# Performance work log

Hardware: AMD Instinct MI355X
Metric: run time of the kernel (lower is better)

## Reference

```python
import jax, jax.numpy as jnp
import numpy as np

B, S, D, H = 2, 1024, 1024, 8
HD = D // H            # head_dim = 128
NBUCKETS = 64          # bucket_size (number of hash buckets)
NEG = -1e30


def setup_inputs() -> dict:
    key = jax.random.key(0)
    ks = jax.random.split(key, 10)
    scale = D ** -0.5
    return {
        "x": jax.random.normal(ks[0], (B, S, D), dtype=jnp.float32),
        "Wq": jax.random.normal(ks[1], (D, D), dtype=jnp.float32) * scale,
        "bq": jnp.zeros((D,), dtype=jnp.float32),
        "Wk": jax.random.normal(ks[2], (D, D), dtype=jnp.float32) * scale,
        "bk": jnp.zeros((D,), dtype=jnp.float32),
        "Wv": jax.random.normal(ks[3], (D, D), dtype=jnp.float32) * scale,
        "bv": jnp.zeros((D,), dtype=jnp.float32),
        "Wo": jax.random.normal(ks[4], (D, D), dtype=jnp.float32) * scale,
        "bo": jnp.zeros((D,), dtype=jnp.float32),
        "hash_proj": jax.random.normal(ks[5], (H, HD, NBUCKETS), dtype=jnp.float32),
    }


def reference(x, Wq, bq, Wk, bk, Wv, bv, Wo, bo, hash_proj):
    b, s, d = x.shape
    n = b * s  # buckets gather (batch, token) pairs jointly -> flatten batch into tokens

    def split_heads(y):  # [B,S,D] -> [H, B*S, HD]
        return y.reshape(b, s, H, HD).transpose(2, 0, 1, 3).reshape(H, n, HD)

    q = split_heads(x @ Wq + bq)
    k = split_heads(x @ Wk + bk)
    v = split_heads(x @ Wv + bv)

    # learned LSH routing: argmax over hash projections per head
    hash_scores = jnp.einsum('hnd,hdf->hnf', q, hash_proj)
    buckets = jnp.argmax(hash_scores, axis=-1)  # [H, N] int

    # per-bucket attention == masked dense attention with same-bucket mask
    dots = jnp.einsum('hnd,hmd->hnm', q, k) / (HD ** 0.5)  # [H,N,N]
    same = buckets[:, :, None] == buckets[:, None, :]
    attn = jax.nn.softmax(jnp.where(same, dots, NEG), axis=-1)
    o = jnp.einsum('hnm,hmd->hnd', attn, v)  # [H,N,HD]

    out = o.reshape(H, b, s, HD).transpose(1, 2, 0, 3).reshape(b, s, d)
    return out @ Wo + bo
```

## Files before the change

kernel.cpp:

```cpp
#include <hip/hip_runtime.h>
#include <stdint.h>

typedef __attribute__((ext_vector_type(8))) short short8;
typedef __attribute__((ext_vector_type(4))) short short4v;
typedef __attribute__((ext_vector_type(4))) float float4v;
typedef unsigned short u16;

#define N_TOK 2048
#define D_MODEL 1024
#define N_HEAD 8
#define HDIM 128
#define N_BUCKET 64
#define WL_CAP 2048
#define ATTN_BLOCKS 384

__device__ __forceinline__ u16 f2bf(float f) {
  uint32_t u = __float_as_uint(f);
  uint32_t r = u + 0x7fffu + ((u >> 16) & 1u);
  return (u16)(r >> 16);
}
__device__ __forceinline__ float bf2f(u16 h) {
  return __uint_as_float(((uint32_t)h) << 16);
}

__device__ __forceinline__ void async_load16(const void* g, void* l) {
  __builtin_amdgcn_global_load_lds(
      (const __attribute__((address_space(1))) void*)g,
      (__attribute__((address_space(3))) void*)l, 16, 0, 0);
}

__device__ __forceinline__ int xcd_swz(int bid, int nwg) {
  return (bid & 7) * (nwg >> 3) + (bid >> 3);
}

__global__ __launch_bounds__(256) void prep_kernel(
    const float* __restrict__ x, const float* __restrict__ Wq,
    const float* __restrict__ Wk, const float* __restrict__ Wv,
    const float* __restrict__ Wo, const float* __restrict__ proj,
    u16* __restrict__ xhi, u16* __restrict__ xlo,
    u16* __restrict__ wqt_hi, u16* __restrict__ wqt_lo, u16* __restrict__ kvt,
    u16* __restrict__ wot, u16* __restrict__ projt_hi,
    u16* __restrict__ projt_lo) {
  const int z = blockIdx.z;
  if (z == 4) {
    int base = (blockIdx.y * 32 + blockIdx.x) * 2048 + threadIdx.x * 8;
    float4v a = *(const float4v*)&x[base];
    float4v b = *(const float4v*)&x[base + 4];
    short8 hi, lo;
#pragma unroll
    for (int j = 0; j < 4; j++) {
      u16 h = f2bf(a[j]);
      hi[j] = (short)h;
      lo[j] = (short)f2bf(a[j] - bf2f(h));
    }
#pragma unroll
    for (int j = 0; j < 4; j++) {
      u16 h = f2bf(b[j]);
      hi[4 + j] = (short)h;
      lo[4 + j] = (short)f2bf(b[j] - bf2f(h));
    }
    *(short8*)&xhi[base] = hi;
    *(short8*)&xlo[base] = lo;
    return;
  }
  __shared__ float tile[32][33];
  int tx = threadIdx.x & 31, ty = threadIdx.x >> 5;
  if (z == 5) {
    if (blockIdx.x >= 2) return;
    const int head = blockIdx.y >> 2;
    const int r0 = (blockIdx.y & 3) * 32;
    const int c0 = blockIdx.x * 32;
    const float* in = proj + (size_t)head * 128 * 64;
#pragma unroll
    for (int i = 0; i < 4; i++) {
      int rl = ty + i * 8;
      tile[rl][tx] = in[(size_t)(r0 + rl) * 64 + c0 + tx];
    }
    __syncthreads();
#pragma unroll
    for (int i = 0; i < 4; i++) {
      int cl = ty + i * 8;
      float v = tile[tx][cl];
      size_t oidx = (size_t)head * 64 * 128 + (size_t)(c0 + cl) * 128 + r0 + tx;
      u16 h = f2bf(v);
      projt_hi[oidx] = h;
      projt_lo[oidx] = f2bf(v - bf2f(h));
    }
    return;
  }
  const float* in = (z == 0) ? Wq : (z == 1) ? Wk : (z == 2) ? Wv : Wo;
  u16* hi = (z == 0) ? wqt_hi
            : (z == 1) ? kvt
            : (z == 2) ? (kvt + (size_t)1024 * 1024) : wot;
  u16* lo = (z == 0) ? wqt_lo : nullptr;
  const int C = 1024, R = 1024;
  int c0 = blockIdx.x * 32, r0 = blockIdx.y * 32;
#pragma unroll
  for (int i = 0; i < 4; i++) {
    int rl = ty + i * 8;
    tile[rl][tx] = in[(size_t)(r0 + rl) * C + c0 + tx];
  }
  __syncthreads();
#pragma unroll
  for (int i = 0; i < 4; i++) {
    int cl = ty + i * 8;
    float v = tile[tx][cl];
    size_t oidx = (size_t)(c0 + cl) * R + r0 + tx;
    u16 h = f2bf(v);
    hi[oidx] = h;
    if (lo) lo[oidx] = f2bf(v - bf2f(h));
  }
}

template <int BM>
__device__ __forceinline__ void stage_tiles2(const u16* A, const u16* Bt,
                                             u16* As, u16* Bs, int bm, int bn,
                                             int K, int ko, int wave, int lane) {
  const int arow = lane >> 2;
  const int acolb = (lane & 3) * 16;
  constexpr int ACH = BM / 16;
  constexpr int PC = (ACH + 8) / 4;
#pragma unroll
  for (int cc = 0; cc < PC; cc++) {
    int idx = wave * PC + cc;
    if (idx < ACH) {
      int row = idx * 16 + arow;
      const char* g = (const char*)A + ((size_t)(bm + row) * K + ko) * 2 + acolb;
      async_load16(g, (char*)As + idx * 1024);
    } else {
      int row = (idx - ACH) * 16 + arow;
      const char* g = (const char*)Bt + ((size_t)(bn + row) * K + ko) * 2 + acolb;
      async_load16(g, (char*)Bs + (idx - ACH) * 1024);
    }
  }
}

template <int BM>
__global__ __launch_bounds__(256) void gemm_bf16_kernel(
    const u16* __restrict__ A, const u16* __restrict__ Bt,
    float* __restrict__ C, const float* __restrict__ bias,
    const float* __restrict__ bias2, u16* __restrict__ kbf,
    u16* __restrict__ vbf, int N, int K, int flags) {
  constexpr int MI = BM / 32;
  __shared__ __align__(16) u16 As[2][BM * 32];
  __shared__ __align__(16) u16 Bs[2][128 * 32];
  const int tid = threadIdx.x;
  const int wave = tid >> 6, lane = tid & 63;
  const int lhi = lane >> 4, llo = lane & 15;
  const int nbn = N >> 7;
  const int bid = xcd_swz(blockIdx.x, gridDim.x);
  const int bm = (bid / nbn) * BM;
  const int bn = (bid % nbn) << 7;
  const int wm = (BM == 128) ? (wave >> 1) * 64 : (wave & 1) * 32;
  const int wn = (BM == 128) ? (wave & 1) * 64 : (wave >> 1) * 64;

  float4v acc[MI][4];
#pragma unroll
  for (int mi = 0; mi < MI; mi++)
#pragma unroll
    for (int ni = 0; ni < 4; ni++)
#pragma unroll
      for (int r = 0; r < 4; r++) acc[mi][ni][r] = 0.f;

  stage_tiles2<BM>(A, Bt, As[0], Bs[0], bm, bn, K, 0, wave, lane);
  __syncthreads();
  const int nk = K >> 5;
  for (int t = 0; t < nk; t++) {
    const int cur = t & 1;
    if (t + 1 < nk)
      stage_tiles2<BM>(A, Bt, As[cur ^ 1], Bs[cur ^ 1], bm, bn, K,
                       (t + 1) << 5, wave, lane);
    short8 af[MI], bfr[4];
#pragma unroll
    for (int i = 0; i < MI; i++)
      af[i] = *(const short8*)&As[cur][(wm + i * 16 + llo) * 32 + lhi * 8];
#pragma unroll
    for (int i = 0; i < 4; i++)
      bfr[i] = *(const short8*)&Bs[cur][(wn + i * 16 + llo) * 32 + lhi * 8];
#pragma unroll
    for (int mi = 0; mi < MI; mi++)
#pragma unroll
      for (int ni = 0; ni < 4; ni++)
        acc[mi][ni] = __builtin_amdgcn_mfma_f32_16x16x32_bf16(af[mi], bfr[ni],
                                                              acc[mi][ni], 0, 0, 0);
    __syncthreads();
  }

#pragma unroll
  for (int mi = 0; mi < MI; mi++)
#pragma unroll
    for (int ni = 0; ni < 4; ni++) {
      int row0 = bm + wm + mi * 16 + lhi * 4;
      int col = bn + wn + ni * 16 + llo;
      if (flags & 8) {
        u16* dst = (col < 1024) ? kbf : vbf;
        int c = col & 1023;
        float bb = (col < 1024) ? bias[c] : bias2[c];
#pragma unroll
        for (int r = 0; r < 4; r++)
          dst[(size_t)(row0 + r) * 1024 + c] = f2bf(acc[mi][ni][r] + bb);
      } else {
        float bb = (flags & 2) ? bias[col] : 0.f;
        float* cp = C + (size_t)row0 * N + col;
#pragma unroll
        for (int r = 0; r < 4; r++) cp[(size_t)r * N] = acc[mi][ni][r] + bb;
      }
    }
}

#define QROW 136
__global__ __launch_bounds__(256) void gemm3_bf16_kernel(
    const u16* __restrict__ A0, const u16* __restrict__ A1,
    const u16* __restrict__ B0, const u16* __restrict__ B1,
    const u16* __restrict__ projt_hi, const u16* __restrict__ projt_lo,
    const float* __restrict__ bias, u16* __restrict__ bf_out,
    int* __restrict__ bucket, int N, int K) {
  constexpr int MI = 2;
  __shared__ __align__(16) u16 S3[2][12288];
  const int tid = threadIdx.x;
  const int wave = tid >> 6, lane = tid & 63;
  const int lhi = lane >> 4, llo = lane & 15;
  const int nbn = N >> 7;
  const int bid = xcd_swz(blockIdx.x, gridDim.x);
  const int bm = (bid / nbn) * 64;
  const int bn = (bid % nbn) << 7;
  const int wm = (wave & 1) * 32;
  const int wn = (wave >> 1) * 64;
  const int arow = lane >> 2;
  const int acolb = (lane & 3) * 16;

  float4v acc[MI][4];
#pragma unroll
  for (int mi = 0; mi < MI; mi++)
#pragma unroll
    for (int ni = 0; ni < 4; ni++)
#pragma unroll
      for (int r = 0; r < 4; r++) acc[mi][ni][r] = 0.f;

  auto stage = [&](int b, int ko) {
    char* base = (char*)&S3[b][0];
#pragma unroll
    for (int cc = 0; cc < 6; cc++) {
      int idx = wave * 6 + cc;
      const u16* src;
      int row;
      char* dst;
      if (idx < 4) {
        src = A0; row = bm + idx * 16 + arow; dst = base + idx * 1024;
      } else if (idx < 8) {
        src = A1; row = bm + (idx - 4) * 16 + arow; dst = base + 4096 + (idx - 4) * 1024;
      } else if (idx < 16) {
        src = B0; row = bn + (idx - 8) * 16 + arow; dst = base + 8192 + (idx - 8) * 1024;
      } else {
        src = B1; row = bn + (idx - 16) * 16 + arow; dst = base + 16384 + (idx - 16) * 1024;
      }
      async_load16((const char*)src + ((size_t)row * K + ko) * 2 + acolb, dst);
    }
  };

  stage(0, 0);
  __syncthreads();
  const int nk = K >> 5;
  for (int t = 0; t < nk; t++) {
    const int cur = t & 1;
    if (t + 1 < nk) stage(cur ^ 1, (t + 1) << 5);
    const u16* Sc = &S3[cur][0];
    short8 afh[MI], afl[MI], bfh[4], bfl[4];
#pragma unroll
    for (int i = 0; i < MI; i++) {
      afh[i] = *(const short8*)&Sc[(wm + i * 16 + llo) * 32 + lhi * 8];
      afl[i] = *(const short8*)&Sc[2048 + (wm + i * 16 + llo) * 32 + lhi * 8];
    }
#pragma unroll
    for (int i = 0; i < 4; i++) {
      bfh[i] = *(const short8*)&Sc[4096 + (wn + i * 16 + llo) * 32 + lhi * 8];
      bfl[i] = *(const short8*)&Sc[8192 + (wn + i * 16 + llo) * 32 + lhi * 8];
    }
#pragma unroll
    for (int mi = 0; mi < MI; mi++)
#pragma unroll
      for (int ni = 0; ni < 4; ni++)
        acc[mi][ni] = __builtin_amdgcn_mfma_f32_16x16x32_bf16(afh[mi], bfh[ni],
                                                              acc[mi][ni], 0, 0, 0);
#pragma unroll
    for (int mi = 0; mi < MI; mi++)
#pragma unroll
      for (int ni = 0; ni < 4; ni++)
        acc[mi][ni] = __builtin_amdgcn_mfma_f32_16x16x32_bf16(afh[mi], bfl[ni],
                                                              acc[mi][ni], 0, 0, 0);
#pragma unroll
    for (int mi = 0; mi < MI; mi++)
#pragma unroll
      for (int ni = 0; ni < 4; ni++)
        acc[mi][ni] = __builtin_amdgcn_mfma_f32_16x16x32_bf16(afl[mi], bfh[ni],
                                                              acc[mi][ni], 0, 0, 0);
    __syncthreads();
  }

  u16* sQh = &S3[0][0];
  u16* sQl = &S3[0][64 * QROW];
#pragma unroll
  for (int mi = 0; mi < MI; mi++)
#pragma unroll
    for (int ni = 0; ni < 4; ni++) {
      int rl0 = wm + mi * 16 + lhi * 4;
      int col = wn + ni * 16 + llo;
      float bb = bias[bn + col];
#pragma unroll
      for (int r = 0; r < 4; r++) {
        float v = acc[mi][ni][r] + bb;
        u16 h = f2bf(v);
        bf_out[(size_t)(bm + rl0 + r) * N + bn + col] = h;
        sQh[(rl0 + r) * QROW + col] = h;
        sQl[(rl0 + r) * QROW + col] = f2bf(v - bf2f(h));
      }
    }
  __syncthreads();

  {
    const int h = bn >> 7;
    const int wm2 = wave * 16;
    short8 qh[4], ql[4];
#pragma unroll
    for (int kf = 0; kf < 4; kf++) {
      qh[kf] = *(const short8*)&sQh[(wm2 + llo) * QROW + kf * 32 + lhi * 8];
      ql[kf] = *(const short8*)&sQl[(wm2 + llo) * QROW + kf * 32 + lhi * 8];
    }
    const u16* ph = projt_hi + (size_t)h * 64 * 128;
    const u16* pl = projt_lo + (size_t)h * 64 * 128;
    float4v sc2[4];
#pragma unroll
    for (int nf = 0; nf < 4; nf++)
#pragma unroll
      for (int r = 0; r < 4; r++) sc2[nf][r] = 0.f;
#pragma unroll
    for (int nf = 0; nf < 4; nf++) {
      int brow = (nf * 16 + llo) * 128;
#pragma unroll
      for (int kf = 0; kf < 4; kf++) {
        short8 bh = *(const short8*)&ph[brow + kf * 32 + lhi * 8];
        short8 bl = *(const short8*)&pl[brow + kf * 32 + lhi * 8];
        sc2[nf] = __builtin_amdgcn_mfma_f32_16x16x32_bf16(qh[kf], bh, sc2[nf], 0, 0, 0);
        sc2[nf] = __builtin_amdgcn_mfma_f32_16x16x32_bf16(qh[kf], bl, sc2[nf], 0, 0, 0);
        sc2[nf] = __builtin_amdgcn_mfma_f32_16x16x32_bf16(ql[kf], bh, sc2[nf], 0, 0, 0);
      }
    }
#pragma unroll
    for (int r = 0; r < 4; r++) {
      float best = sc2[0][r];
      int bi = llo;
#pragma unroll
      for (int nf = 1; nf < 4; nf++) {
        float v = sc2[nf][r];
        if (v > best) { best = v; bi = nf * 16 + llo; }
      }
#pragma unroll
      for (int o = 1; o < 16; o <<= 1) {
        float ov = __shfl_xor(best, o);
        int oi = __shfl_xor(bi, o);
        if (ov > best || (ov == best && oi < bi)) { best = ov; bi = oi; }
      }
      if (llo == 0) bucket[h * N_TOK + bm + wm2 + lhi * 4 + r] = bi;
    }
  }
}

__global__ __launch_bounds__(64) void bucket_count_kernel(
    const int* __restrict__ bucket, int* __restrict__ counts) {
  int hb = blockIdx.x;
  int h = hb >> 6, b = hb & 63;
  int lane = threadIdx.x;
  int cnt = 0;
  for (int t = 0; t < N_TOK; t += 64) {
    bool match = bucket[h * N_TOK + t + lane] == b;
    unsigned long long mask = __ballot(match);
    cnt += __popcll(mask);
  }
  if (lane == 0) counts[hb] = cnt;
}

__global__ __launch_bounds__(512) void build_wl_kernel(
    const int* __restrict__ counts, int* __restrict__ offsets,
    int* __restrict__ wl, int* __restrict__ wl_count) {
  __shared__ int sc[512];
  int tid = threadIdx.x;
  int cnt = counts[tid];
  sc[tid] = cnt;
  __syncthreads();
  for (int o = 1; o < 512; o <<= 1) {
    int v = (tid >= o) ? sc[tid - o] : 0;
    __syncthreads();
    sc[tid] += v;
    __syncthreads();
  }
  offsets[tid] = sc[tid] - cnt;
  __syncthreads();
  int nq = (cnt + 15) >> 4;
  sc[tid] = nq;
  __syncthreads();
  for (int o = 1; o < 512; o <<= 1) {
    int v = (tid >= o) ? sc[tid - o] : 0;
    __syncthreads();
    sc[tid] += v;
    __syncthreads();
  }
  int base = sc[tid] - nq;
  int h = tid >> 6, b = tid & 63;
  for (int i = 0; i < nq; i++) wl[base + i] = (h << 13) | (b << 7) | i;
  if (tid == 511) wl_count[0] = sc[511];
}

__global__ __launch_bounds__(64) void bucket_fill_kernel(
    const int* __restrict__ bucket, const int* __restrict__ offsets,
    int* __restrict__ perm) {
  int hb = blockIdx.x;
  int h = hb >> 6, b = hb & 63;
  int lane = threadIdx.x;
  int base = offsets[hb];
  for (int t = 0; t < N_TOK; t += 64) {
    int tok = t + lane;
    bool match = bucket[h * N_TOK + tok] == b;
    unsigned long long mask = __ballot(match);
    if (match) {
      int pos = base + __popcll(mask & ((1ull << lane) - 1ull));
      perm[pos] = tok;
    }
    base += __popcll(mask);
  }
}

__global__ __launch_bounds__(256) void gather_vt_kernel(
    const u16* __restrict__ vbb, const int* __restrict__ perm,
    u16* __restrict__ Vts) {
  __shared__ u16 lds[64][72];
  int bid = blockIdx.x;
  int h = bid >> 6;
  int ptile = (bid & 63) >> 1;
  int d0 = (bid & 1) * 64;
  int pos0 = ptile * 64;
  int t = threadIdx.x;
#pragma unroll
  for (int i = 0; i < 2; i++) {
    int unit = t + 256 * i;
    int p = unit >> 3, seg = unit & 7;
    int tok = perm[h * N_TOK + pos0 + p];
    short8 v = *(const short8*)&vbb[(size_t)tok * D_MODEL + h * HDIM + d0 + seg * 8];
    *(short8*)&lds[p][seg * 8] = v;
  }
  __syncthreads();
#pragma unroll
  for (int i = 0; i < 8; i++) {
    int unit = t + 256 * i;
    int drow = unit >> 5, pp = unit & 31;
    uint32_t val = (uint32_t)lds[2 * pp][drow] |
                   ((uint32_t)lds[2 * pp + 1][drow] << 16);
    uint32_t* dst = (uint32_t*)&Vts[(size_t)(h * HDIM + d0 + drow) * N_TOK + pos0];
    dst[pp] = val;
  }
}

__global__ __launch_bounds__(256) void attn_bucket_kernel(
    const u16* __restrict__ qbb, const u16* __restrict__ kbb,
    const u16* __restrict__ Vts, const int* __restrict__ perm,
    const int* __restrict__ offsets, const int* __restrict__ counts,
    const int* __restrict__ wl, const int* __restrict__ wl_count,
    u16* __restrict__ ob) {
  const int wave = threadIdx.x >> 6, lane = threadIdx.x & 63;
  const int lhi = lane >> 4, llo = lane & 15;
  const int wslot = blockIdx.x * 4 + wave;
  const int NW = ATTN_BLOCKS * 4;
  const int cnt = wl_count[0];
  __shared__ __align__(16) u16 P_lds[4][16][64];
  const float scale = 0.08838834764831845f;

  for (int e = wslot; e < cnt; e += NW) {
    int ent = wl[e];
    int h = ent >> 13, qt = ent & 127;
    int hb = (h << 6) | ((ent >> 7) & 63);
    int off = offsets[hb];
    int bs = counts[hb];
    int offh = off - h * N_TOK;
    int qbase = qt * 16;

    int qr = qbase + llo;
    int tokq = perm[off + min(qr, bs - 1)];
    const u16* qrow = &qbb[(size_t)tokq * D_MODEL + h * HDIM];
    short8 qf[4];
#pragma unroll
    for (int kf = 0; kf < 4; kf++)
      qf[kf] = *(const short8*)&qrow[kf * 32 + lhi * 8];

    float m[4], l[4];
#pragma unroll
    for (int r = 0; r < 4; r++) { m[r] = -INFINITY; l[r] = 0.f; }
    float4v accO[8];
#pragma unroll
    for (int d = 0; d < 8; d++)
#pragma unroll
      for (int r = 0; r < 4; r++) accO[d][r] = 0.f;

    for (int c0 = 0; c0 < bs; c0 += 64) {
      float4v scv[4];
#pragma unroll
      for (int nf = 0; nf < 4; nf++)
#pragma unroll
        for (int r = 0; r < 4; r++) scv[nf][r] = 0.f;
#pragma unroll
      for (int nf = 0; nf < 4; nf++) {
        int kcol = c0 + nf * 16 + llo;
        int tokk = perm[off + min(kcol, bs - 1)];
        const u16* krow = &kbb[(size_t)tokk * D_MODEL + h * HDIM];
#pragma unroll
        for (int kf = 0; kf < 4; kf++) {
          short8 kfr = *(const short8*)&krow[kf * 32 + lhi * 8];
          scv[nf] = __builtin_amdgcn_mfma_f32_16x16x32_bf16(qf[kf], kfr, scv[nf], 0, 0, 0);
        }
      }

      float tmax[4];
#pragma unroll
      for (int r = 0; r < 4; r++) tmax[r] = -INFINITY;
#pragma unroll
      for (int nf = 0; nf < 4; nf++) {
        bool valid = (c0 + nf * 16 + llo) < bs;
#pragma unroll
        for (int r = 0; r < 4; r++) {
          float v = valid ? scv[nf][r] * scale : -1e30f;
          scv[nf][r] = v;
          tmax[r] = fmaxf(tmax[r], v);
        }
      }
#pragma unroll
      for (int r = 0; r < 4; r++)
#pragma unroll
        for (int o = 1; o < 16; o <<= 1)
          tmax[r] = fmaxf(tmax[r], __shfl_xor(tmax[r], o));

      float resc[4], psum[4];
#pragma unroll
      for (int r = 0; r < 4; r++) {
        float mn = fmaxf(m[r], tmax[r]);
        resc[r] = __expf(m[r] - mn);
        m[r] = mn;
        psum[r] = 0.f;
      }
#pragma unroll
      for (int nf = 0; nf < 4; nf++)
#pragma unroll
        for (int r = 0; r < 4; r++) {
          float p = __expf(scv[nf][r] - m[r]);
          psum[r] += p;
          P_lds[wave][lhi * 4 + r][nf * 16 + llo] = f2bf(p);
        }
#pragma unroll
      for (int r = 0; r < 4; r++) {
#pragma unroll
        for (int o = 1; o < 16; o <<= 1) psum[r] += __shfl_xor(psum[r], o);
        l[r] = l[r] * resc[r] + psum[r];
      }
#pragma unroll
      for (int d = 0; d < 8; d++)
#pragma unroll
        for (int r = 0; r < 4; r++) accO[d][r] *= resc[r];

      asm volatile("s_waitcnt lgkmcnt(0)" ::: "memory");
      short8 pf[2];
#pragma unroll
      for (int k2 = 0; k2 < 2; k2++)
        pf[k2] = *(const short8*)&P_lds[wave][llo][k2 * 32 + lhi * 8];
#pragma unroll
      for (int d = 0; d < 8; d++)
#pragma unroll
        for (int k2 = 0; k2 < 2; k2++) {
          short8 vfr = *(const short8*)&Vts[(size_t)(h * HDIM + d * 16 + llo) * N_TOK +
                                            offh + c0 + k2 * 32 + lhi * 8];
          accO[d] = __builtin_amdgcn_mfma_f32_16x16x32_bf16(pf[k2], vfr, accO[d], 0, 0, 0);
        }
      asm volatile("" ::: "memory");
    }

#pragma unroll
    for (int r = 0; r < 4; r++) {
      int rl = qbase + lhi * 4 + r;
      if (rl < bs) {
        int tok = perm[off + rl];
        float inv = 1.f / l[r];
#pragma unroll
        for (int d = 0; d < 8; d++)
          ob[(size_t)tok * D_MODEL + h * HDIM + d * 16 + llo] = f2bf(accO[d][r] * inv);
      }
    }
  }
}

extern "C" void kernel_launch(void* const* d_in, const int* in_sizes, int n_in,
                              void* d_out, int out_size, void* d_ws, size_t ws_size,
                              hipStream_t stream) {
  const float* x  = (const float*)d_in[0];
  const float* Wq = (const float*)d_in[1];
  const float* bq = (const float*)d_in[2];
  const float* Wk = (const float*)d_in[3];
  const float* bk = (const float*)d_in[4];
  const float* Wv = (const float*)d_in[5];
  const float* bv = (const float*)d_in[6];
  const float* Wo = (const float*)d_in[7];
  const float* bo = (const float*)d_in[8];
  const float* hp = (const float*)d_in[9];
  float* out = (float*)d_out;

  char* ws = (char*)d_ws;
  size_t off = 0;
  auto alloc = [&](size_t b) {
    char* p = ws + off;
    off += (b + 255) & ~(size_t)255;
    return p;
  };

  const int N = N_TOK, D = D_MODEL;
  u16* xhi    = (u16*)alloc((size_t)N * D * 2);
  u16* xlo    = (u16*)alloc((size_t)N * D * 2);
  u16* wqt_hi = (u16*)alloc((size_t)D * D * 2);
  u16* wqt_lo = (u16*)alloc((size_t)D * D * 2);
  u16* kvt    = (u16*)alloc((size_t)2 * D * D * 2);
  u16* wot    = (u16*)alloc((size_t)D * D * 2);
  u16* pjt_hi = (u16*)alloc((size_t)N_HEAD * 64 * 128 * 2);
  u16* pjt_lo = (u16*)alloc((size_t)N_HEAD * 64 * 128 * 2);
  u16* qbb    = (u16*)alloc((size_t)N * D * 2);
  u16* kbb    = (u16*)alloc((size_t)N * D * 2);
  u16* vbb    = (u16*)alloc((size_t)N * D * 2);
  u16* Vts    = (u16*)alloc((size_t)N_HEAD * HDIM * N * 2 + 256);
  int* bucket = (int*)alloc((size_t)N_HEAD * N * 4);
  int* counts = (int*)alloc(512 * 4);
  int* offs   = (int*)alloc(512 * 4);
  int* perm   = (int*)alloc((size_t)N_HEAD * N * 4);
  int* wl     = (int*)alloc(WL_CAP * 4);
  int* wlcnt  = (int*)alloc(256);
  u16* ob     = (u16*)alloc((size_t)N * D * 2);

  prep_kernel<<<dim3(32, 32, 6), 256, 0, stream>>>(
      x, Wq, Wk, Wv, Wo, hp, xhi, xlo, wqt_hi, wqt_lo, kvt, wot, pjt_hi, pjt_lo);

  gemm3_bf16_kernel<<<(N / 64) * (D / 128), 256, 0, stream>>>(
      xhi, xlo, wqt_hi, wqt_lo, pjt_hi, pjt_lo, bq, qbb, bucket, D, D);
  gemm_bf16_kernel<64><<<(N / 64) * (2 * D / 128), 256, 0, stream>>>(
      xhi, kvt, nullptr, bk, bv, kbb, vbb, 2 * D, D, 2 | 8);

  bucket_count_kernel<<<512, 64, 0, stream>>>(bucket, counts);
  build_wl_kernel<<<1, 512, 0, stream>>>(counts, offs, wl, wlcnt);
  bucket_fill_kernel<<<512, 64, 0, stream>>>(bucket, offs, perm);
  gather_vt_kernel<<<512, 256, 0, stream>>>(vbb, perm, Vts);

  attn_bucket_kernel<<<ATTN_BLOCKS, 256, 0, stream>>>(
      qbb, kbb, Vts, perm, offs, counts, wl, wlcnt, ob);

  gemm_bf16_kernel<64><<<(N / 64) * (D / 128), 256, 0, stream>>>(
      ob, wot, out, bo, nullptr, nullptr, nullptr, D, D, 2);

  (void)in_sizes; (void)n_in; (void)out_size; (void)ws_size;
}
```

Before: 122.1 us.

## Merge Q-projection-with-hashing and KV projection GEMMs into one interleaved launch

Replaces the separate Q GEMM (split-precision, with fused LSH bucket argmax) and the K/V GEMM with a single 768-block kernel. Blocks are interleaved 1:2 by blockIdx mod 3, so the costlier 3-MFMA Q tiles share the GPU with the cheaper single-pass KV tiles. This removes one kernel launch and the tail gap between the two GEMMs, and lets the two workloads overlap across CUs. The cost is a larger kernel with two code paths, which may raise register pressure and reduce occupancy.

```diff
diff --git a/kernel.cpp b/kernel.cpp
--- a/kernel.cpp
+++ b/kernel.cpp
@@ -209,159 +209,218 @@
 }
 
 #define QROW 136
-__global__ __launch_bounds__(256) void gemm3_bf16_kernel(
+__global__ __launch_bounds__(256) void proj_gemm_kernel(
     const u16* __restrict__ A0, const u16* __restrict__ A1,
     const u16* __restrict__ B0, const u16* __restrict__ B1,
-    const u16* __restrict__ projt_hi, const u16* __restrict__ projt_lo,
-    const float* __restrict__ bias, u16* __restrict__ bf_out,
-    int* __restrict__ bucket, int N, int K) {
-  constexpr int MI = 2;
+    const u16* __restrict__ kvt, const u16* __restrict__ projt_hi,
+    const u16* __restrict__ projt_lo, const float* __restrict__ bq,
+    const float* __restrict__ bk, const float* __restrict__ bv,
+    u16* __restrict__ qbb, int* __restrict__ bucket,
+    u16* __restrict__ kbf, u16* __restrict__ vbf) {
   __shared__ __align__(16) u16 S3[2][12288];
   const int tid = threadIdx.x;
   const int wave = tid >> 6, lane = tid & 63;
   const int lhi = lane >> 4, llo = lane & 15;
-  const int nbn = N >> 7;
-  const int bid = xcd_swz(blockIdx.x, gridDim.x);
-  const int bm = (bid / nbn) * 64;
-  const int bn = (bid % nbn) << 7;
-  const int wm = (wave & 1) * 32;
-  const int wn = (wave >> 1) * 64;
   const int arow = lane >> 2;
   const int acolb = (lane & 3) * 16;
-
-  float4v acc[MI][4];
-#pragma unroll
-  for (int mi = 0; mi < MI; mi++)
-#pragma unroll
-    for (int ni = 0; ni < 4; ni++)
-#pragma unroll
-      for (int r = 0; r < 4; r++) acc[mi][ni][r] = 0.f;
-
-  auto stage = [&](int b, int ko) {
-    char* base = (char*)&S3[b][0];
-#pragma unroll
-    for (int cc = 0; cc < 6; cc++) {
-      int idx = wave * 6 + cc;
-      const u16* src;
-      int row;
-      char* dst;
-      if (idx < 4) {
-        src = A0; row = bm + idx * 16 + arow; dst = base + idx * 1024;
-      } else if (idx < 8) {
-        src = A1; row = bm + (idx - 4) * 16 + arow; dst = base + 4096 + (idx - 4) * 1024;
-      } else if (idx < 16) {
-        src = B0; row = bn + (idx - 8) * 16 + arow; dst = base + 8192 + (idx - 8) * 1024;
-      } else {
-        src = B1; row = bn + (idx - 16) * 16 + arow; dst = base + 16384 + (idx - 16) * 1024;
-      }
-      async_load16((const char*)src + ((size_t)row * K + ko) * 2 + acolb, dst);
-    }
-  };
-
-  stage(0, 0);
-  __syncthreads();
-  const int nk = K >> 5;
-  for (int t = 0; t < nk; t++) {
-    const int cur = t & 1;
-    if (t + 1 < nk) stage(cur ^ 1, (t + 1) << 5);
-    const u16* Sc = &S3[cur][0];
-    short8 afh[MI], afl[MI], bfh[4], bfl[4];
-#pragma unroll
-    for (int i = 0; i < MI; i++) {
-      afh[i] = *(const short8*)&Sc[(wm + i * 16 + llo) * 32 + lhi * 8];
-      afl[i] = *(const short8*)&Sc[2048 + (wm + i * 16 + llo) * 32 + lhi * 8];
-    }
-#pragma unroll
-    for (int i = 0; i < 4; i++) {
-      bfh[i] = *(const short8*)&Sc[4096 + (wn + i * 16 + llo) * 32 + lhi * 8];
-      bfl[i] = *(const short8*)&Sc[8192 + (wn + i * 16 + llo) * 32 + lhi * 8];
-    }
-#pragma unroll
-    for (int mi = 0; mi < MI; mi++)
+  const int K = 1024;
+  const int b = blockIdx.x;
+  const int cls = b % 3;
+
+  if (cls == 0) {
+    const int bid = b / 3;
+    const int bm = (bid >> 3) * 64;
+    const int bn = (bid & 7) << 7;
+    const int wm = (wave & 1) * 32;
+    const int wn = (wave >> 1) * 64;
+
+    float4v acc[2][4];
+#pragma unroll
+    for (int mi = 0; mi < 2; mi++)
 #pragma unroll
       for (int ni = 0; ni < 4; ni++)
-        acc[mi][ni] = __builtin_amdgcn_mfma_f32_16x16x32_bf16(afh[mi], bfh[ni],
-                                                              acc[mi][ni], 0, 0, 0);
-#pragma unroll
-    for (int mi = 0; mi < MI; mi++)
+#pragma unroll
+        for (int r = 0; r < 4; r++) acc[mi][ni][r] = 0.f;
+
+    auto stage = [&](int bb2, int ko) {
+      char* base = (char*)&S3[bb2][0];
+#pragma unroll
+      for (int cc = 0; cc < 6; cc++) {
+        int idx = wave * 6 + cc;
+        const u16* src;
+        int row;
+        char* dst;
+        if (idx < 4) {
+          src = A0; row = bm + idx * 16 + arow; dst = base + idx * 1024;
+        } else if (idx < 8) {
+          src = A1; row = bm + (idx - 4) * 16 + arow; dst = base + 4096 + (idx - 4) * 1024;
+        } else if (idx < 16) {
+          src = B0; row = bn + (idx - 8) * 16 + arow; dst = base + 8192 + (idx - 8) * 1024;
+        } else {
+          src = B1; row = bn + (idx - 16) * 16 + arow; dst = base + 16384 + (idx - 16) * 1024;
+        }
+        async_load16((const char*)src + ((size_t)row * K + ko) * 2 + acolb, dst);
+      }
+    };
+
+    stage(0, 0);
+    __syncthreads();
+    for (int t = 0; t < 32; t++) {
+      const int cur = t & 1;
+      if (t + 1 < 32) stage(cur ^ 1, (t + 1) << 5);
+      const u16* Sc = &S3[cur][0];
+      short8 afh[2], afl[2], bfh[4], bfl[4];
+#pragma unroll
+      for (int i = 0; i < 2; i++) {
+        afh[i] = *(const short8*)&Sc[(wm + i * 16 + llo) * 32 + lhi * 8];
+        afl[i] = *(const short8*)&Sc[2048 + (wm + i * 16 + llo) * 32 + lhi * 8];
+      }
+#pragma unroll
+      for (int i = 0; i < 4; i++) {
+        bfh[i] = *(const short8*)&Sc[4096 + (wn + i * 16 + llo) * 32 + lhi * 8];
+        bfl[i] = *(const short8*)&Sc[8192 + (wn + i * 16 + llo) * 32 + lhi * 8];
+      }
+#pragma unroll
+      for (int mi = 0; mi < 2; mi++)
+#pragma unroll
+        for (int ni = 0; ni < 4; ni++)
+          acc[mi][ni] = __builtin_amdgcn_mfma_f32_16x16x32_bf16(afh[mi], bfh[ni],
+                                                                acc[mi][ni], 0, 0, 0);
+#pragma unroll
+      for (int mi = 0; mi < 2; mi++)
+#pragma unroll
+        for (int ni = 0; ni < 4; ni++)
+          acc[mi][ni] = __builtin_amdgcn_mfma_f32_16x16x32_bf16(afh[mi], bfl[ni],
+                                                                acc[mi][ni], 0, 0, 0);
+#pragma unroll
+      for (int mi = 0; mi < 2; mi++)
+#pragma unroll
+        for (int ni = 0; ni < 4; ni++)
+          acc[mi][ni] = __builtin_amdgcn_mfma_f32_16x16x32_bf16(afl[mi], bfh[ni],
+                                                                acc[mi][ni], 0, 0, 0);
+      __syncthreads();
+    }
+
+    u16* sQh = &S3[0][0];
+    u16* sQl = &S3[0][64 * QROW];
+#pragma unroll
+    for (int mi = 0; mi < 2; mi++)
+#pragma unroll
+      for (int ni = 0; ni < 4; ni++) {
+        int rl0 = wm + mi * 16 + lhi * 4;
+        int col = wn + ni * 16 + llo;
+        float bb = bq[bn + col];
+#pragma unroll
+        for (int r = 0; r < 4; r++) {
+          float v = acc[mi][ni][r] + bb;
+          u16 h = f2bf(v);
+          qbb[(size_t)(bm + rl0 + r) * 1024 + bn + col] = h;
+          sQh[(rl0 + r) * QROW + col] = h;
+          sQl[(rl0 + r) * QROW + col] = f2bf(v - bf2f(h));
+        }
+      }
+    __syncthreads();
+
+    {
+      const int h = bn >> 7;
+      const int wm2 = wave * 16;
+      short8 qh[4], ql[4];
+#pragma unroll
+      for (int kf = 0; kf < 4; kf++) {
+        qh[kf] = *(const short8*)&sQh[(wm2 + llo) * QROW + kf * 32 + lhi * 8];
+        ql[kf] = *(const short8*)&sQl[(wm2 + llo) * QROW + kf * 32 + lhi * 8];
+      }
+      const u16* ph = projt_hi + (size_t)h * 64 * 128;
+      const u16* pl = projt_lo + (size_t)h * 64 * 128;
+      float4v sc2[4];
+#pragma unroll
+      for (int nf = 0; nf < 4; nf++)
+#pragma unroll
+        for (int r = 0; r < 4; r++) sc2[nf][r] = 0.f;
+#pragma unroll
+      for (int nf = 0; nf < 4; nf++) {
+        int brow = (nf * 16 + llo) * 128;
+#pragma unroll
+        for (int kf = 0; kf < 4; kf++) {
+          short8 bh = *(const short8*)&ph[brow + kf * 32 + lhi * 8];
+          short8 bl = *(const short8*)&pl[brow + kf * 32 + lhi * 8];
+          sc2[nf] = __builtin_amdgcn_mfma_f32_16x16x32_bf16(qh[kf], bh, sc2[nf], 0, 0, 0);
+          sc2[nf] = __builtin_amdgcn_mfma_f32_16x16x32_bf16(qh[kf], bl, sc2[nf], 0, 0, 0);
+          sc2[nf] = __builtin_amdgcn_mfma_f32_16x16x32_bf16(ql[kf], bh, sc2[nf], 0, 0, 0);
+        }
+      }
+#pragma unroll
+      for (int r = 0; r < 4; r++) {
+        float best = sc2[0][r];
+        int bi = llo;
+#pragma unroll
+        for (int nf = 1; nf < 4; nf++) {
+          float v = sc2[nf][r];
+          if (v > best) { best = v; bi = nf * 16 + llo; }
+        }
+#pragma unroll
+        for (int o = 1; o < 16; o <<= 1) {
+          float ov = __shfl_xor(best, o);
+          int oi = __shfl_xor(bi, o);
+          if (ov > best || (ov == best && oi < bi)) { best = ov; bi = oi; }
+        }
+        if (llo == 0) bucket[h * N_TOK + bm + wm2 + lhi * 4 + r] = bi;
+      }
+    }
+  } else {
+    const int bid2 = (b / 3) * 2 + (cls - 1);
+    const int bm = (bid2 >> 4) * 64;
+    const int bn = (bid2 & 15) << 7;
+    const int wm = (wave & 1) * 32;
+    const int wn = (wave >> 1) * 64;
+
+    float4v acc[2][4];
+#pragma unroll
+    for (int mi = 0; mi < 2; mi++)
 #pragma unroll
       for (int ni = 0; ni < 4; ni++)
-        acc[mi][ni] = __builtin_amdgcn_mfma_f32_16x16x32_bf16(afh[mi], bfl[ni],
-                                                              acc[mi][ni], 0, 0, 0);
-#pragma unroll
-    for (int mi = 0; mi < MI; mi++)
-#pragma unroll
-      for (int ni = 0; ni < 4; ni++)
-        acc[mi][ni] = __builtin_amdgcn_mfma_f32_16x16x32_bf16(afl[mi], bfh[ni],
-                                                              acc[mi][ni], 0, 0, 0);
-    __syncthreads();
-  }
-
-  u16* sQh = &S3[0][0];
-  u16* sQl = &S3[0][64 * QROW];
-#pragma unroll
-  for (int mi = 0; mi < MI; mi++)
-#pragma unroll
-    for (int ni = 0; ni < 4; ni++) {
-      int rl0 = wm + mi * 16 + lhi * 4;
-      int col = wn + ni * 16 + llo;
-      float bb = bias[bn + col];
-#pragma unroll
-      for (int r = 0; r < 4; r++) {
-        float v = acc[mi][ni][r] + bb;
-        u16 h = f2bf(v);
-        bf_out[(size_t)(bm + rl0 + r) * N + bn + col] = h;
-        sQh[(rl0 + r) * QROW + col] = h;
-        sQl[(rl0 + r) * QROW + col] = f2bf(v - bf2f(h));
-      }
-    }
-  __syncthreads();
-
-  {
-    const int h = bn >> 7;
-    const int wm2 = wave * 16;
-    short8 qh[4], ql[4];
-#pragma unroll
-    for (int kf = 0; kf < 4; kf++) {
-      qh[kf] = *(const short8*)&sQh[(wm2 + llo) * QROW + kf * 32 + lhi * 8];
-      ql[kf] = *(const short8*)&sQl[(wm2 + llo) * QROW + kf * 32 + lhi * 8];
-    }
-    const u16* ph = projt_hi + (size_t)h * 64 * 128;
-    const u16* pl = projt_lo + (size_t)h * 64 * 128;
-    float4v sc2[4];
-#pragma unroll
-    for (int nf = 0; nf < 4; nf++)
-#pragma unroll
-      for (int r = 0; r < 4; r++) sc2[nf][r] = 0.f;
-#pragma unroll
-    for (int nf = 0; nf < 4; nf++) {
-      int brow = (nf * 16 + llo) * 128;
-#pragma unroll
-      for (int kf = 0; kf < 4; kf++) {
-        short8 bh = *(const short8*)&ph[brow + kf * 32 + lhi * 8];
-        short8 bl = *(const short8*)&pl[brow + kf * 32 + lhi * 8];
-        sc2[nf] = __builtin_amdgcn_mfma_f32_16x16x32_bf16(qh[kf], bh, sc2[nf], 0, 0, 0);
-        sc2[nf] = __builtin_amdgcn_mfma_f32_16x16x32_bf16(qh[kf], bl, sc2[nf], 0, 0, 0);
-        sc2[nf] = __builtin_amdgcn_mfma_f32_16x16x32_bf16(ql[kf], bh, sc2[nf], 0, 0, 0);
-      }
-    }
-#pragma unroll
-    for (int r = 0; r < 4; r++) {
-      float best = sc2[0][r];
-      int bi = llo;
-#pragma unroll
-      for (int nf = 1; nf < 4; nf++) {
-        float v = sc2[nf][r];
-        if (v > best) { best = v; bi = nf * 16 + llo; }
-      }
-#pragma unroll
-      for (int o = 1; o < 16; o <<= 1) {
-        float ov = __shfl_xor(best, o);
-        int oi = __shfl_xor(bi, o);
-        if (ov > best || (ov == best && oi < bi)) { best = ov; bi = oi; }
-      }
-      if (llo == 0) bucket[h * N_TOK + bm + wm2 + lhi * 4 + r] = bi;
-    }
+#pragma unroll
+        for (int r = 0; r < 4; r++) acc[mi][ni][r] = 0.f;
+
+    stage_tiles2<64>(A0, kvt, &S3[0][0], &S3[0][4096], bm, bn, K, 0, wave, lane);
+    __syncthreads();
+    for (int t = 0; t < 32; t++) {
+      const int cur = t & 1;
+      if (t + 1 < 32)
+        stage_tiles2<64>(A0, kvt, &S3[0][(cur ^ 1) * 2048],
+                         &S3[0][4096 + (cur ^ 1) * 4096], bm, bn, K,
+                         (t + 1) << 5, wave, lane);
+      const u16* Ac = &S3[0][cur * 2048];
+      const u16* Bc = &S3[0][4096 + cur * 4096];
+      short8 af[2], bfr[4];
+#pragma unroll
+      for (int i = 0; i < 2; i++)
+        af[i] = *(const short8*)&Ac[(wm + i * 16 + llo) * 32 + lhi * 8];
+#pragma unroll
+      for (int i = 0; i < 4; i++)
+        bfr[i] = *(const short8*)&Bc[(wn + i * 16 + llo) * 32 + lhi * 8];
+#pragma unroll
+      for (int mi = 0; mi < 2; mi++)
+#pragma unroll
+        for (int ni = 0; ni < 4; ni++)
+          acc[mi][ni] = __builtin_amdgcn_mfma_f32_16x16x32_bf16(af[mi], bfr[ni],
+                                                                acc[mi][ni], 0, 0, 0);
+      __syncthreads();
+    }
+
+#pragma unroll
+    for (int mi = 0; mi < 2; mi++)
+#pragma unroll
+      for (int ni = 0; ni < 4; ni++) {
+        int row0 = bm + wm + mi * 16 + lhi * 4;
+        int col = bn + wn + ni * 16 + llo;
+        u16* dst = (col < 1024) ? kbf : vbf;
+        int c = col & 1023;
+        float bb = (col < 1024) ? bk[c] : bv[c];
+#pragma unroll
+        for (int r = 0; r < 4; r++)
+          dst[(size_t)(row0 + r) * 1024 + c] = f2bf(acc[mi][ni][r] + bb);
+      }
   }
 }
 
@@ -640,10 +699,9 @@
   prep_kernel<<<dim3(32, 32, 6), 256, 0, stream>>>(
       x, Wq, Wk, Wv, Wo, hp, xhi, xlo, wqt_hi, wqt_lo, kvt, wot, pjt_hi, pjt_lo);
 
-  gemm3_bf16_kernel<<<(N / 64) * (D / 128), 256, 0, stream>>>(
-      xhi, xlo, wqt_hi, wqt_lo, pjt_hi, pjt_lo, bq, qbb, bucket, D, D);
-  gemm_bf16_kernel<64><<<(N / 64) * (2 * D / 128), 256, 0, stream>>>(
-      xhi, kvt, nullptr, bk, bv, kbb, vbb, 2 * D, D, 2 | 8);
+  proj_gemm_kernel<<<768, 256, 0, stream>>>(
+      xhi, xlo, wqt_hi, wqt_lo, kvt, pjt_hi, pjt_lo, bq, bk, bv,
+      qbb, bucket, kbb, vbb);
 
   bucket_count_kernel<<<512, 64, 0, stream>>>(bucket, counts);
   build_wl_kernel<<<1, 512, 0, stream>>>(counts, offs, wl, wlcnt);
```

Result: faster. 109.8 us (-10.1%).
